# Kernel optimization log

Measured on AMD Instinct MI355X. Metric: run time of the kernel, lower is better.

## Reference

```python
import jax, jax.numpy as jnp
import numpy as np
from jax import lax


def setup_inputs() -> dict:
    key = jax.random.key(0)
    ks = jax.random.split(key, 8)
    B, L, H = 2, 1024, 2048
    E = 2
    d = H * E            # d_inner = 4096
    S = 16               # state_dim
    R = 128              # dt_rank = ceil(H / 16)
    sc = lambda fan_in: 1.0 / np.sqrt(fan_in)
    return {
        "x": jax.random.normal(ks[0], (B, L, H), jnp.float32),
        "W_in": jax.random.normal(ks[1], (H, 2 * d), jnp.float32) * sc(H),
        "conv_w": jax.random.normal(ks[2], (d, 1, 3), jnp.float32) * sc(3),
        "conv_b": jnp.zeros((d,), jnp.float32),
        "W_x": jax.random.normal(ks[3], (d, R + 2 * S), jnp.float32) * sc(d),
        "W_dt": jax.random.normal(ks[4], (R, d), jnp.float32) * sc(R),
        "b_dt": jnp.zeros((d,), jnp.float32),
        "A_log": jnp.log(jnp.tile(jnp.arange(1, S + 1, dtype=jnp.float32), (d, 1))),
        "D": jnp.ones((d,), jnp.float32),
        "W_out": jax.random.normal(ks[5], (d, H), jnp.float32) * sc(d),
    }


def reference(x, W_in, conv_w, conv_b, W_x, W_dt, b_dt, A_log, D, W_out):
    d = conv_b.shape[0]
    S = A_log.shape[1]
    R = W_dt.shape[0]
    # in_proj and gate split
    xz = x @ W_in                              # [B, L, 2d]
    xp, z = jnp.split(xz, 2, axis=-1)          # each [B, L, d]
    # depthwise conv1d (kernel 3, pad 1)
    xc = lax.conv_general_dilated(
        jnp.transpose(xp, (0, 2, 1)), conv_w, (1,), [(1, 1)],
        feature_group_count=d, dimension_numbers=("NCH", "OIH", "NCH"))
    xc = jnp.transpose(xc + conv_b[None, :, None], (0, 2, 1))  # [B, L, d]
    xc = jax.nn.silu(xc)
    # x_proj -> dt, B, C
    x_dbl = xc @ W_x                           # [B, L, R + 2S]
    dt_in = x_dbl[..., :R]
    Bm = x_dbl[..., R:R + S]                   # [B, L, S]
    Cm = x_dbl[..., R + S:]                    # [B, L, S]
    dt = jax.nn.softplus(dt_in @ W_dt + b_dt)  # [B, L, d]
    A = -jnp.exp(A_log)                        # [d, S]

    def step(h, ins):
        u_t, dt_t, B_t, C_t = ins              # [B,d], [B,d], [B,S], [B,S]
        dA = jnp.exp(dt_t[:, :, None] * A)     # [B, d, S]
        h = dA * h + dt_t[:, :, None] * B_t[:, None, :] * u_t[:, :, None]
        y_t = jnp.einsum("bds,bs->bd", h, C_t)
        return h, y_t

    h0 = jnp.zeros((x.shape[0], d, S), xc.dtype)
    xsT = (jnp.swapaxes(xc, 0, 1), jnp.swapaxes(dt, 0, 1),
           jnp.swapaxes(Bm, 0, 1), jnp.swapaxes(Cm, 0, 1))
    _, yT = lax.scan(step, h0, xsT)            # yT: [L, B, d]
    y = jnp.swapaxes(yT, 0, 1) + xc * D        # skip connection
    y = y * jax.nn.silu(z)                     # gate
    return y @ W_out                           # [B, L, H]
```

## Files before the change

### kernel.cpp

```cpp
#include <hip/hip_runtime.h>
#include <hip/hip_bf16.h>


using u16 = unsigned short;
typedef __bf16 bf16x8 __attribute__((ext_vector_type(8)));
typedef float f32x4 __attribute__((ext_vector_type(4)));
typedef u16 u16x8 __attribute__((ext_vector_type(8)));
typedef u16 u16x4 __attribute__((ext_vector_type(4)));

#define NCHUNK 16
#define CLEN   64
#define SWZ(row, q) ((q) ^ (((row) >> 1) & 3))

__device__ __forceinline__ float bf2f(u16 u) {
    union { unsigned int i; float f; } v; v.i = ((unsigned int)u) << 16; return v.f;
}
__device__ __forceinline__ u16 f2bf(float f) {
    union { float f; unsigned int i; } v; v.f = f;
    unsigned int x = v.i;
    return (u16)((x + 0x7FFFu + ((x >> 16) & 1u)) >> 16);
}

__device__ __forceinline__ float* hloc_ptr(u16* xzbase, int i) {
    return reinterpret_cast<float*>(xzbase + (size_t)(i >> 11) * 8192) + (i & 2047);
}
__device__ __forceinline__ float* hin_ptr(u16* xzbase, int i) {
    return reinterpret_cast<float*>(xzbase + (size_t)((i >> 11) + 1024) * 8192) + (i & 2047);
}

__global__ void detect_dtype(const u16* __restrict__ xraw, int* __restrict__ flag) {
    __shared__ int cnt[256];
    const int tid = threadIdx.x;
    int plausible = 0;
    for (int i = tid; i < 4096; i += 256) {
        const u16 v = xraw[2 * i];
        const int e = (v >> 7) & 0xFF;
        plausible += (e >= 100 && e <= 145) ? 1 : 0;
    }
    cnt[tid] = plausible;
    __syncthreads();
    for (int s = 128; s > 0; s >>= 1) {
        if (tid < s) cnt[tid] += cnt[tid + s];
        __syncthreads();
    }
    if (tid == 0) *flag = (cnt[0] > 2458) ? 1 : 0;
}

__device__ __forceinline__ void cvt_seg8(const void* src, u16* dst, int i8,
                                         bool isbf) {
    if (isbf) {
        *(u16x8*)&dst[i8 * 8] = *((const u16x8*)src + i8);
    } else {
        const float* f = (const float*)src + i8 * 8;
        u16x8 o;
#pragma unroll
        for (int j = 0; j < 8; j++) o[j] = f2bf(f[j]);
        *(u16x8*)&dst[i8 * 8] = o;
    }
}
__global__ void cvt_fused(const void* __restrict__ x_raw, u16* __restrict__ xcan,
                          const void* __restrict__ cw_raw, u16* __restrict__ cw_c,
                          const void* __restrict__ cb_raw, u16* __restrict__ cb_c,
                          const void* __restrict__ bdt_raw, u16* __restrict__ bdt_c,
                          const void* __restrict__ Alog_raw, u16* __restrict__ Alog_c,
                          const void* __restrict__ D_raw, u16* __restrict__ D_c,
                          const int* __restrict__ flag) {
    const bool isbf = (*flag != 0);
    int blk = blockIdx.x;
    const int tid = threadIdx.x;
    if (blk < 2048) { cvt_seg8(x_raw, xcan, blk * 256 + tid, isbf); return; }
    blk -= 2048;
    if (blk < 6)  { cvt_seg8(cw_raw, cw_c, blk * 256 + tid, isbf); return; }
    blk -= 6;
    if (blk < 2)  { cvt_seg8(cb_raw, cb_c, blk * 256 + tid, isbf); return; }
    blk -= 2;
    if (blk < 2)  { cvt_seg8(bdt_raw, bdt_c, blk * 256 + tid, isbf); return; }
    blk -= 2;
    if (blk < 32) { cvt_seg8(Alog_raw, Alog_c, blk * 256 + tid, isbf); return; }
    blk -= 32;
    cvt_seg8(D_raw, D_c, blk * 256 + tid, isbf);
}

__device__ __forceinline__ void tr_tile(const void* in, u16* out, int R, int C,
                                        int bx, int by, int tx, int ty, bool isbf,
                                        u16 (*tile)[34]) {
    const int c0 = bx * 32, r0 = by * 64;
    const int cp = tx & 15, rh = tx >> 4;
#pragma unroll
    for (int i = 0; i < 4; i++) {
        const int row = ty + rh * 8 + i * 16;
        const size_t idx = (size_t)(r0 + row) * C + c0 + cp * 2;
        if (isbf) {
            union { unsigned int u; u16 h[2]; } p;
            p.u = *reinterpret_cast<const unsigned int*>(&((const u16*)in)[idx]);
            tile[row][cp * 2] = p.h[0];
            tile[row][cp * 2 + 1] = p.h[1];
        } else {
            const float2 f = *reinterpret_cast<const float2*>(&((const float*)in)[idx]);
            tile[row][cp * 2] = f2bf(f.x);
            tile[row][cp * 2 + 1] = f2bf(f.y);
        }
    }
    __syncthreads();
#pragma unroll
    for (int i = 0; i < 4; i++) {
        const int w = ty + i * 8;
        union { u16 h[2]; unsigned int u; } p;
        p.h[0] = tile[2 * tx][w];
        p.h[1] = tile[2 * tx + 1][w];
        *reinterpret_cast<unsigned int*>(&out[(size_t)(c0 + w) * R + r0 + 2 * tx]) = p.u;
    }
}
__global__ void transpose_fused(const void* __restrict__ Wi, u16* __restrict__ WiT,
                                const void* __restrict__ Wo, u16* __restrict__ WoT,
                                const void* __restrict__ Wd, u16* __restrict__ WdT,
                                const void* __restrict__ Wx, u16* __restrict__ WxT,
                                const int* __restrict__ flag) {
    __shared__ u16 tile[64][34];
    const bool isbf = (*flag != 0);
    const int tx = threadIdx.x, ty = threadIdx.y;
    int blk = blockIdx.x;
    if (blk < 8192) { tr_tile(Wi, WiT, 2048, 8192, blk % 256, blk / 256, tx, ty, isbf, tile); return; }
    blk -= 8192;
    if (blk < 4096) { tr_tile(Wo, WoT, 4096, 2048, blk % 64, blk / 64, tx, ty, isbf, tile); return; }
    blk -= 4096;
    if (blk < 256)  { tr_tile(Wd, WdT, 128, 4096, blk % 128, blk / 128, tx, ty, isbf, tile); return; }
    blk -= 256;
    tr_tile(Wx, WxT, 4096, 160, blk % 5, blk / 5, tx, ty, isbf, tile);
}

template <int BM, int BN, int THR>
__device__ __forceinline__ void stage_ring(const u16* __restrict__ Ab,
                                           const u16* __restrict__ Bb,
                                           int K, int k0, u16* dst, int tid)
{
    constexpr int CHA = BM * 4, CHB = BN * 4;
    static_assert(CHA % THR == 0 && CHB % THR == 0, "chunk/thread mismatch");
#pragma unroll
    for (int it = 0; it < CHA / THR; it++) {
        const int c = it * THR + tid;
        const int row = c >> 2, kc = SWZ(row, c & 3);
        __builtin_amdgcn_global_load_lds(
            (const __attribute__((address_space(1))) void*)(Ab + (size_t)row * K + k0 + kc * 8),
            (__attribute__((address_space(3))) void*)(dst + c * 8), 16, 0, 0);
    }
#pragma unroll
    for (int it = 0; it < CHB / THR; it++) {
        const int c = it * THR + tid;
        const int row = c >> 2, kc = SWZ(row, c & 3);
        __builtin_amdgcn_global_load_lds(
            (const __attribute__((address_space(1))) void*)(Bb + (size_t)row * K + k0 + kc * 8),
            (__attribute__((address_space(3))) void*)(dst + BM * 32 + c * 8), 16, 0, 0);
    }
}

template <int BM, int BN, int WM, int WN, int MODE, int RING>
__global__ __launch_bounds__(64 * WM * WN, 2) void gemm_ring(
    const u16* __restrict__ A, const u16* __restrict__ Bt, void* __restrict__ C,
    const int* __restrict__ oflagp, int M, int N, int K)
{
    constexpr int THR = 64 * WM * WN;
    constexpr int MT  = BM / (WM * 16);
    constexpr int NT  = BN / (WN * 16);
    constexpr int NPH = 2;
    constexpr int GM  = MT / NPH;
    constexpr int STG = (BM + BN) * 32;
    constexpr int LPS = (BM + BN) * 4 / THR;
    constexpr int AHEAD = RING - 1;
    static_assert((BM * 4) % THR == 0 && (BN * 4) % THR == 0, "chunk split");
    static_assert(MT % NPH == 0, "MT must split into NPH phases");
    extern __shared__ u16 smem[];

    const int tid  = threadIdx.x;
    const int lane = tid & 63;
    const int wave = tid >> 6;
    const int wm = wave / WN, wn = wave % WN;
    const int q  = lane >> 4;
    const int n0 = blockIdx.x * BN;
    const int m0 = blockIdx.y * BM;
    const int Kchunk = K / gridDim.z;
    const int kbeg = blockIdx.z * Kchunk;
    const int NTILE = Kchunk >> 5;

    const u16* Ab = A  + (size_t)m0 * K + kbeg;
    const u16* Bb = Bt + (size_t)n0 * K + kbeg;

#pragma unroll
    for (int s = 0; s < AHEAD; s++)
        stage_ring<BM, BN, THR>(Ab, Bb, K, s * 32, smem + s * STG, tid);

    f32x4 acc[MT][NT];
#pragma unroll
    for (int mi = 0; mi < MT; mi++)
#pragma unroll
        for (int ni = 0; ni < NT; ni++)
            acc[mi][ni] = (f32x4){0.f, 0.f, 0.f, 0.f};

    const int arow = wm * (MT * 16) + (lane & 15);
    const int brow = wn * (NT * 16) + (lane & 15);

    int cbuf = 0;
    int pbuf = AHEAD % RING;

    for (int t = 0; t < NTILE; t++) {
        const int tp = t + AHEAD;
        if (tp < NTILE) {
            stage_ring<BM, BN, THR>(Ab, Bb, K, tp * 32, smem + pbuf * STG, tid);
            asm volatile("s_waitcnt vmcnt(%0)" :: "n"(AHEAD * LPS) : "memory");
        } else if (tp == NTILE) {
            asm volatile("s_waitcnt vmcnt(%0)" :: "n"((AHEAD - 1) * LPS) : "memory");
        } else if (tp == NTILE + 1) {
            asm volatile("s_waitcnt vmcnt(%0)" :: "n"(((AHEAD >= 2) ? (AHEAD - 2) : 0) * LPS) : "memory");
        } else {
            asm volatile("s_waitcnt vmcnt(0)" ::: "memory");
        }
        __builtin_amdgcn_s_barrier();

        const u16* As = smem + cbuf * STG;
        const u16* Bs = As + BM * 32;
        bf16x8 bfr[NT];
#pragma unroll
        for (int ni = 0; ni < NT; ni++) {
            const int r = brow + ni * 16;
            bfr[ni] = *reinterpret_cast<const bf16x8*>(&Bs[r * 32 + SWZ(r, q) * 8]);
        }
#pragma unroll
        for (int g = 0; g < NPH; g++) {
            bf16x8 af[GM];
#pragma unroll
            for (int i = 0; i < GM; i++) {
                const int r = arow + (g * GM + i) * 16;
                af[i] = *reinterpret_cast<const bf16x8*>(&As[r * 32 + SWZ(r, q) * 8]);
            }
            __builtin_amdgcn_s_setprio(1);
#pragma unroll
            for (int i = 0; i < GM; i++)
#pragma unroll
                for (int ni = 0; ni < NT; ni++)
                    acc[g * GM + i][ni] = __builtin_amdgcn_mfma_f32_16x16x32_bf16(
                        af[i], bfr[ni], acc[g * GM + i][ni], 0, 0, 0);
            __builtin_amdgcn_s_setprio(0);
            __builtin_amdgcn_sched_barrier(0);
            __builtin_amdgcn_s_barrier();
        }
        cbuf = (cbuf + 1 == RING) ? 0 : cbuf + 1;
        pbuf = (pbuf + 1 == RING) ? 0 : pbuf + 1;
    }

    int oflag = 1;
    if constexpr (MODE == 1) oflag = *oflagp;

    const int rb = m0 + wm * (MT * 16) + (q << 2);
    const int cb = n0 + wn * (NT * 16) + (lane & 15);
#pragma unroll
    for (int mi = 0; mi < MT; mi++) {
#pragma unroll
        for (int ni = 0; ni < NT; ni++) {
            const int col = cb + ni * 16;
#pragma unroll
            for (int r = 0; r < 4; r++) {
                const int row = rb + mi * 16 + r;
                const float v = acc[mi][ni][r];
                if constexpr (MODE == 0) {
                    ((u16*)C)[(size_t)row * N + col] = f2bf(v);
                } else if constexpr (MODE == 2) {
                    ((float*)C)[((size_t)blockIdx.z * M + row) * N + col] = v;
                } else {
                    if (oflag) ((u16*)C)[(size_t)row * N + col] = f2bf(v);
                    else       ((float*)C)[(size_t)row * N + col] = v;
                }
            }
        }
    }
}

__global__ void reduce_out(const float* __restrict__ part, void* __restrict__ out,
                           const int* __restrict__ flag) {
    const int idx = blockIdx.x * 256 + threadIdx.x;
    const int i4 = idx * 4;
    const float4 a = *(const float4*)&part[i4];
    const float4 b = *(const float4*)&part[(size_t)4194304 + i4];
    if (*flag) {
        u16x4 o;
        o[0] = f2bf(a.x + b.x); o[1] = f2bf(a.y + b.y);
        o[2] = f2bf(a.z + b.z); o[3] = f2bf(a.w + b.w);
        *(u16x4*)&((u16*)out)[i4] = o;
    } else {
        float4 s = {a.x + b.x, a.y + b.y, a.z + b.z, a.w + b.w};
        *(float4*)&((float*)out)[i4] = s;
    }
}

template <int BM, int BN, int BK, int WR, int WC, int MT, int NT, int MODE>
__global__ __launch_bounds__(256) void gemm_bt(
    const u16* __restrict__ A, const u16* __restrict__ Bt,
    void* __restrict__ C, const u16* __restrict__ bias,
    const int* __restrict__ oflagp,
    int M, int N, int K)
{
    static_assert(BK == 32, "BK=32 (one 16x16x32 MFMA k-slab)");
    __shared__ u16 As[BM * BK];
    __shared__ u16 Bs[BN * BK];

    const int tid  = threadIdx.x;
    const int lane = tid & 63;
    const int wave = tid >> 6;
    const int wm = wave / WC, wn = wave % WC;

    const int m0 = blockIdx.y * BM;
    const int n0 = blockIdx.x * BN;
    const int Kchunk = K / gridDim.z;
    const int kbeg = blockIdx.z * Kchunk;
    const int kend = kbeg + Kchunk;

    f32x4 acc[MT][NT];
#pragma unroll
    for (int mi = 0; mi < MT; mi++)
#pragma unroll
        for (int ni = 0; ni < NT; ni++)
            acc[mi][ni] = (f32x4){0.f, 0.f, 0.f, 0.f};

    const int q = lane >> 4;
    const int arow = wm * MT * 16 + (lane & 15);
    const int brow = wn * NT * 16 + (lane & 15);

    constexpr int CHA = BM * 4;
    constexpr int CHB = BN * 4;

    for (int k0 = kbeg; k0 < kend; k0 += BK) {
        __syncthreads();
#pragma unroll
        for (int it = 0; it < (CHA + 255) / 256; it++) {
            const int c = it * 256 + tid;
            if (CHA % 256 == 0 || c < CHA) {
                const int row = c >> 2, kc = SWZ(row, c & 3);
                const u16* gp = &A[(size_t)(m0 + row) * K + k0 + kc * 8];
                __builtin_amdgcn_global_load_lds(
                    (const __attribute__((address_space(1))) void*)gp,
                    (__attribute__((address_space(3))) void*)&As[c * 8], 16, 0, 0);
            }
        }
#pragma unroll
        for (int it = 0; it < (CHB + 255) / 256; it++) {
            const int c = it * 256 + tid;
            if (CHB % 256 == 0 || c < CHB) {
                const int row = c >> 2, kc = SWZ(row, c & 3);
                const u16* gp = &Bt[(size_t)(n0 + row) * K + k0 + kc * 8];
                __builtin_amdgcn_global_load_lds(
                    (const __attribute__((address_space(1))) void*)gp,
                    (__attribute__((address_space(3))) void*)&Bs[c * 8], 16, 0, 0);
            }
        }
        __syncthreads();

        bf16x8 af[MT], bfr[NT];
#pragma unroll
        for (int mi = 0; mi < MT; mi++) {
            const int row = arow + mi * 16;
            af[mi] = *reinterpret_cast<const bf16x8*>(&As[row * BK + SWZ(row, q) * 8]);
        }
#pragma unroll
        for (int ni = 0; ni < NT; ni++) {
            const int row = brow + ni * 16;
            bfr[ni] = *reinterpret_cast<const bf16x8*>(&Bs[row * BK + SWZ(row, q) * 8]);
        }
#pragma unroll
        for (int mi = 0; mi < MT; mi++)
#pragma unroll
            for (int ni = 0; ni < NT; ni++)
                acc[mi][ni] = __builtin_amdgcn_mfma_f32_16x16x32_bf16(
                    af[mi], bfr[ni], acc[mi][ni], 0, 0, 0);
    }

    const int rb = m0 + wm * MT * 16 + ((lane >> 4) << 2);
    const int cb = n0 + wn * NT * 16 + (lane & 15);
#pragma unroll
    for (int mi = 0; mi < MT; mi++) {
#pragma unroll
        for (int ni = 0; ni < NT; ni++) {
            const int col = cb + ni * 16;
#pragma unroll
            for (int r = 0; r < 4; r++) {
                const int row = rb + mi * 16 + r;
                const float v = acc[mi][ni][r];
                if constexpr (MODE == 0) {
                    ((u16*)C)[(size_t)row * N + col] = f2bf(v);
                } else if constexpr (MODE == 5) {
                    ((float*)C)[((size_t)blockIdx.z * M + row) * N + col] = v;
                }
            }
        }
    }
}

__global__ void reduce_xdbl(const float* __restrict__ part,
                            float* __restrict__ x_dbl, u16* __restrict__ dtin) {
    const int idx = blockIdx.x * 256 + threadIdx.x;
    const int row = idx / 160, col = idx - row * 160;
    float s = 0.f;
#pragma unroll
    for (int z = 0; z < 16; z++) s += part[(size_t)z * (2048 * 160) + idx];
    x_dbl[idx] = s;
    if (col < 128) dtin[row * 128 + col] = f2bf(s);
}

__global__ __launch_bounds__(256) void dt_gemm(
    const u16* __restrict__ A,
    const u16* __restrict__ Bt,
    u16* __restrict__ C,
    const u16* __restrict__ bias)
{
    __shared__ ulong4 smem_raw[2048];
    u16* As = (u16*)smem_raw;
    u16* Bs = As + 64 * 128;
    float* Cs = (float*)smem_raw;

    const int tid  = threadIdx.x;
    const int lane = tid & 63;
    const int wave = tid >> 6;
    const int n0 = blockIdx.x * 64;
    const int m0 = blockIdx.y * 64;

#pragma unroll
    for (int it = 0; it < 4; it++) {
        const int c = it * 256 + tid;
        const int row = c >> 4, cc = (c & 15) ^ (row & 7);
        const u16* gp = &A[(size_t)(m0 + row) * 128 + cc * 8];
        __builtin_amdgcn_global_load_lds(
            (const __attribute__((address_space(1))) void*)gp,
            (__attribute__((address_space(3))) void*)&As[c * 8], 16, 0, 0);
    }
#pragma unroll
    for (int it = 0; it < 4; it++) {
        const int c = it * 256 + tid;
        const int row = c >> 4, cc = (c & 15) ^ (row & 7);
        const u16* gp = &Bt[(size_t)(n0 + row) * 128 + cc * 8];
        __builtin_amdgcn_global_load_lds(
            (const __attribute__((address_space(1))) void*)gp,
            (__attribute__((address_space(3))) void*)&Bs[c * 8], 16, 0, 0);
    }
    __syncthreads();

    const int q  = lane >> 4;
    const int ar = wave * 16 + (lane & 15);
    f32x4 acc[4];
#pragma unroll
    for (int ni = 0; ni < 4; ni++) acc[ni] = (f32x4){0.f, 0.f, 0.f, 0.f};

#pragma unroll
    for (int kk = 0; kk < 4; kk++) {
        const int cA = kk * 4 + q;
        const bf16x8 af = *reinterpret_cast<const bf16x8*>(
            &As[(ar * 16 + (cA ^ (ar & 7))) * 8]);
#pragma unroll
        for (int ni = 0; ni < 4; ni++) {
            const int br = ni * 16 + (lane & 15);
            const bf16x8 bfr = *reinterpret_cast<const bf16x8*>(
                &Bs[(br * 16 + (cA ^ (br & 7))) * 8]);
            acc[ni] = __builtin_amdgcn_mfma_f32_16x16x32_bf16(af, bfr, acc[ni], 0, 0, 0);
        }
    }
    __syncthreads();

#pragma unroll
    for (int ni = 0; ni < 4; ni++) {
        const int col = ni * 16 + (lane & 15);
#pragma unroll
        for (int r = 0; r < 4; r++) {
            const int rowl = wave * 16 + q * 4 + r;
            Cs[rowl * 68 + col] = acc[ni][r];
        }
    }
    __syncthreads();

#pragma unroll
    for (int p = 0; p < 4; p++) {
        const int rowl = p * 16 + (tid >> 4);
        const int c0 = (tid & 15) * 4;
        float4 v = *reinterpret_cast<const float4*>(&Cs[rowl * 68 + c0]);
        float* vp = reinterpret_cast<float*>(&v);
        u16x4 o;
#pragma unroll
        for (int j = 0; j < 4; j++) {
            const float x = vp[j] + bf2f(bias[n0 + c0 + j]);
            o[j] = f2bf(fmaxf(x, 0.f) + __logf(1.f + __expf(-fabsf(x))));
        }
        *reinterpret_cast<u16x4*>(&C[(size_t)(m0 + rowl) * 4096 + n0 + c0]) = o;
    }
}

__global__ void conv_silu(const u16* __restrict__ xz, const u16* __restrict__ conv_w,
                          const u16* __restrict__ conv_b, u16* __restrict__ xc) {
    const int idx = blockIdx.x * 256 + threadIdx.x;
    const int row = idx >> 9, c0 = (idx & 511) * 8;
    const int l = row & 1023;

    u16 wcat[24];
    *(u16x8*)&wcat[0]  = *(const u16x8*)&conv_w[c0 * 3];
    *(u16x8*)&wcat[8]  = *(const u16x8*)&conv_w[c0 * 3 + 8];
    *(u16x8*)&wcat[16] = *(const u16x8*)&conv_w[c0 * 3 + 16];
    const u16x8 bv = *(const u16x8*)&conv_b[c0];
    const u16x8 x0 = *(const u16x8*)&xz[(size_t)row * 8192 + c0];
    u16x8 xm = {}, xp = {};
    if (l > 0)    xm = *(const u16x8*)&xz[(size_t)(row - 1) * 8192 + c0];
    if (l < 1023) xp = *(const u16x8*)&xz[(size_t)(row + 1) * 8192 + c0];

    u16x8 out;
#pragma unroll
    for (int i = 0; i < 8; i++) {
        float v = bf2f(wcat[3 * i]) * bf2f(xm[i])
                + bf2f(wcat[3 * i + 1]) * bf2f(x0[i])
                + bf2f(wcat[3 * i + 2]) * bf2f(xp[i])
                + bf2f(bv[i]);
        v = v / (1.f + __expf(-v));
        out[i] = f2bf(v);
    }
    *(u16x8*)&xc[(size_t)row * 4096 + c0] = out;
}

__global__ __launch_bounds__(256) void scan_p1(
    const u16* __restrict__ dt, const u16* __restrict__ xc,
    const float* __restrict__ x_dbl, const u16* __restrict__ A_log,
    float* __restrict__ Parr, u16* __restrict__ xzbase)
{
    __shared__ float Bsm[CLEN][16];
    const int tid = threadIdx.x;
    const int nc = blockIdx.x, cg = blockIdx.y, b = blockIdx.z;
    const int ch = cg * 256 + tid;
    const size_t row0 = (size_t)b * 1024 + nc * CLEN;

    {
        const int t = tid >> 2, q = tid & 3;
        const float4 v = *(const float4*)&x_dbl[(row0 + t) * 160 + 128 + q * 4];
        *(float4*)&Bsm[t][q * 4] = v;
    }
    __syncthreads();

    float A_s[16], h[16];
#pragma unroll
    for (int s = 0; s < 16; s++) {
        A_s[s] = -__expf(bf2f(A_log[ch * 16 + s]));
        h[s] = 0.f;
    }
    float Sdt = 0.f;

    float dt_v = bf2f(dt[row0 * 4096 + ch]);
    float u_v  = bf2f(xc[row0 * 4096 + ch]);
    for (int t = 0; t < CLEN; t++) {
        const int tn = (t + 1 < CLEN) ? t + 1 : t;
        const float dt_n = bf2f(dt[(row0 + tn) * 4096 + ch]);
        const float u_n  = bf2f(xc[(row0 + tn) * 4096 + ch]);
        const float dtu = dt_v * u_v;
        Sdt += dt_v;
        const f32x4* Brow = (const f32x4*)&Bsm[t][0];
        const f32x4 B0 = Brow[0], B1 = Brow[1], B2 = Brow[2], B3 = Brow[3];
#pragma unroll
        for (int s = 0; s < 16; s++) {
            const float Bs_ = (s < 4 ? B0[s & 3] : s < 8 ? B1[s & 3] : s < 12 ? B2[s & 3] : B3[s & 3]);
            const float dA = __expf(dt_v * A_s[s]);
            h[s] = dA * h[s] + dtu * Bs_;
        }
        dt_v = dt_n; u_v = u_n;
    }
    const int i0 = (((b * NCHUNK + nc) * 4096) + ch) * 16;
    float* pp = &Parr[i0];
    float* hp = hloc_ptr(xzbase, i0);
#pragma unroll
    for (int s4 = 0; s4 < 4; s4++) {
        float4 pq, hq;
        pq.x = __expf(A_s[4 * s4 + 0] * Sdt);
        pq.y = __expf(A_s[4 * s4 + 1] * Sdt);
        pq.z = __expf(A_s[4 * s4 + 2] * Sdt);
        pq.w = __expf(A_s[4 * s4 + 3] * Sdt);
        hq.x = h[4 * s4 + 0]; hq.y = h[4 * s4 + 1];
        hq.z = h[4 * s4 + 2]; hq.w = h[4 * s4 + 3];
        *(float4*)&pp[4 * s4] = pq;
        *(float4*)&hp[4 * s4] = hq;
    }
}

__global__ __launch_bounds__(256) void scan_p2(
    const float* __restrict__ Parr, u16* __restrict__ xzbase)
{
    const int tid = threadIdx.x;
    const int lane = tid & 63, wave = tid >> 6;
    const int blk = blockIdx.x;
    const int b = blk >> 8, cg = blk & 255;
    const int c_local = lane & 3, s = lane >> 2;
    const int ch = cg * 16 + wave * 4 + c_local;

    float Pv[NCHUNK], hl[NCHUNK];
#pragma unroll
    for (int c = 0; c < NCHUNK; c++) {
        const int i = (((b * NCHUNK + c) * 4096) + ch) * 16 + s;
        Pv[c] = Parr[i];
        hl[c] = *hloc_ptr(xzbase, i);
    }
    float hin = 0.f;
#pragma unroll
    for (int c = 0; c < NCHUNK; c++) {
        const int i = (((b * NCHUNK + c) * 4096) + ch) * 16 + s;
        *hin_ptr(xzbase, i) = hin;
        hin = Pv[c] * hin + hl[c];
    }
}

__global__ __launch_bounds__(256) void scan_p3(
    const u16* __restrict__ dt, const u16* __restrict__ xc,
    const float* __restrict__ x_dbl, const u16* __restrict__ xz,
    const u16* __restrict__ A_log, const u16* __restrict__ Dp,
    u16* __restrict__ yg, u16* __restrict__ xzbase)
{
    __shared__ float BCs[CLEN][32];
    const int tid = threadIdx.x;
    const int nc = blockIdx.x, cg = blockIdx.y, b = blockIdx.z;
    const int ch = cg * 256 + tid;
    const size_t row0 = (size_t)b * 1024 + nc * CLEN;

#pragma unroll
    for (int it = 0; it < 2; it++) {
        const int c = it * 256 + tid;
        const int t = c >> 3, q = c & 7;
        const float4 v = *(const float4*)&x_dbl[(row0 + t) * 160 + 128 + q * 4];
        *(float4*)&BCs[t][q * 4] = v;
    }
    __syncthreads();

    float A_s[16], h[16];
    const int i0 = (((b * NCHUNK + nc) * 4096) + ch) * 16;
    {
        const float* hp = hin_ptr(xzbase, i0);
#pragma unroll
        for (int s4 = 0; s4 < 4; s4++) {
            const float4 hq = *(const float4*)&hp[4 * s4];
            h[4 * s4 + 0] = hq.x; h[4 * s4 + 1] = hq.y;
            h[4 * s4 + 2] = hq.z; h[4 * s4 + 3] = hq.w;
        }
    }
#pragma unroll
    for (int s = 0; s < 16; s++)
        A_s[s] = -__expf(bf2f(A_log[ch * 16 + s]));
    const float D_ch = bf2f(Dp[ch]);

    float dt_v = bf2f(dt[row0 * 4096 + ch]);
    float u_v  = bf2f(xc[row0 * 4096 + ch]);
    float z_v  = bf2f(xz[row0 * 8192 + 4096 + ch]);
    for (int t = 0; t < CLEN; t++) {
        const int tn = (t + 1 < CLEN) ? t + 1 : t;
        const size_t rn = row0 + tn;
        const float dt_n = bf2f(dt[rn * 4096 + ch]);
        const float u_n  = bf2f(xc[rn * 4096 + ch]);
        const float z_n  = bf2f(xz[rn * 8192 + 4096 + ch]);
        const float dtu = dt_v * u_v;

        const f32x4* Row = (const f32x4*)&BCs[t][0];
        const f32x4 B0 = Row[0], B1 = Row[1], B2 = Row[2], B3 = Row[3];
        const f32x4 C0 = Row[4], C1 = Row[5], C2 = Row[6], C3 = Row[7];

        float y0 = 0.f, y1 = 0.f, y2 = 0.f, y3 = 0.f;
#pragma unroll
        for (int s = 0; s < 16; s++) {
            const float Bs_ = (s < 4 ? B0[s & 3] : s < 8 ? B1[s & 3] : s < 12 ? B2[s & 3] : B3[s & 3]);
            const float Cs_ = (s < 4 ? C0[s & 3] : s < 8 ? C1[s & 3] : s < 12 ? C2[s & 3] : C3[s & 3]);
            const float dA = __expf(dt_v * A_s[s]);
            h[s] = dA * h[s] + dtu * Bs_;
            const float hc = h[s] * Cs_;
            if ((s & 3) == 0) y0 += hc; else if ((s & 3) == 1) y1 += hc;
            else if ((s & 3) == 2) y2 += hc; else y3 += hc;
        }
        const float y = (y0 + y1) + (y2 + y3);
        const float silu_z = z_v / (1.f + __expf(-z_v));
        yg[(row0 + t) * 4096 + ch] = f2bf((y + u_v * D_ch) * silu_z);
        dt_v = dt_n; u_v = u_n; z_v = z_n;
    }
}

extern "C" void kernel_launch(void* const* d_in, const int* in_sizes, int n_in,
                              void* d_out, int out_size, void* d_ws, size_t ws_size,
                              hipStream_t stream)
{
    const void* x_raw      = d_in[0];
    const void* W_in_raw   = d_in[1];
    const void* conv_w_raw = d_in[2];
    const void* conv_b_raw = d_in[3];
    const void* W_x_raw    = d_in[4];
    const void* W_dt_raw   = d_in[5];
    const void* b_dt_raw   = d_in[6];
    const void* A_log_raw  = d_in[7];
    const void* D_raw      = d_in[8];
    const void* W_out_raw  = d_in[9];

    char* ws = (char*)d_ws;
    size_t off = 0;
    auto alloc = [&](size_t bytes) { char* p = ws + off; off += (bytes + 255) & ~(size_t)255; return p; };
    int*   flag   = (int*)  alloc(4);
    u16*   W_inT  = (u16*)  alloc(8192ULL * 2048 * 2);
    u16*   W_outT = (u16*)  alloc(2048ULL * 4096 * 2);
    u16*   W_dtT  = (u16*)  alloc(4096ULL * 128 * 2);
    u16*   W_xT   = (u16*)  alloc(160ULL * 4096 * 2);
    u16*   xz     = (u16*)  alloc(2048ULL * 8192 * 2);
    u16*   xc     = (u16*)  alloc(2048ULL * 4096 * 2);
    float* x_dbl  = (float*)alloc(2048ULL * 160 * 4);
    u16*   dtin   = (u16*)  alloc(2048ULL * 128 * 2);
    u16*   yg     = (u16*)  alloc(2048ULL * 4096 * 2);
    u16*   xcan   = (u16*)  alloc(2048ULL * 2048 * 2);
    float* xdblp  = (float*)alloc(16ULL * 2048 * 160 * 4);
    u16*   cw_c   = (u16*)  alloc(12288 * 2);
    u16*   cb_c   = (u16*)  alloc(4096 * 2);
    u16*   bdt_c  = (u16*)  alloc(4096 * 2);
    u16*   Alog_c = (u16*)  alloc(65536 * 2);
    u16*   D_c    = (u16*)  alloc(4096 * 2);
    u16*   dtv    = (u16*)W_inT;
    float* Parr   = (float*)xcan;
    float* outp   = (float*)W_inT;

    detect_dtype<<<1, 256, 0, stream>>>((const u16*)x_raw, flag);
    cvt_fused<<<2048 + 6 + 2 + 2 + 32 + 2, 256, 0, stream>>>(
        x_raw, xcan, conv_w_raw, cw_c, conv_b_raw, cb_c, b_dt_raw, bdt_c,
        A_log_raw, Alog_c, D_raw, D_c, flag);

    transpose_fused<<<8192 + 4096 + 256 + 320, dim3(32, 8), 0, stream>>>(
        W_in_raw, W_inT, W_out_raw, W_outT, W_dt_raw, W_dtT, W_x_raw, W_xT, flag);

    (void)hipFuncSetAttribute(
        reinterpret_cast<const void*>(&gemm_ring<256, 128, 2, 2, 0, 3>),
        hipFuncAttributeMaxDynamicSharedMemorySize, 73728);
    gemm_ring<256, 128, 2, 2, 0, 3><<<dim3(8192 / 128, 2048 / 256, 1), 256, 73728, stream>>>(
        xcan, W_inT, xz, nullptr, 2048, 8192, 2048);

    conv_silu<<<(2048 * 512) / 256, 256, 0, stream>>>(xz, cw_c, cb_c, xc);

    gemm_bt<64, 160, 32, 4, 1, 1, 10, 5>
        <<<dim3(1, 2048 / 64, 16), 256, 0, stream>>>(xc, W_xT, xdblp, nullptr, nullptr, 2048, 160, 4096);

    reduce_xdbl<<<(2048 * 160) / 256, 256, 0, stream>>>(xdblp, x_dbl, dtin);

    dt_gemm<<<dim3(4096 / 64, 2048 / 64), 256, 0, stream>>>(dtin, W_dtT, dtv, bdt_c);

    scan_p1<<<dim3(NCHUNK, 16, 2), 256, 0, stream>>>(dtv, xc, x_dbl, Alog_c, Parr, xz);
    scan_p2<<<512, 256, 0, stream>>>(Parr, xz);
    scan_p3<<<dim3(NCHUNK, 16, 2), 256, 0, stream>>>(dtv, xc, x_dbl, xz, Alog_c, D_c, yg, xz);

    (void)hipFuncSetAttribute(
        reinterpret_cast<const void*>(&gemm_ring<128, 128, 2, 2, 2, 4>),
        hipFuncAttributeMaxDynamicSharedMemorySize, 65536);
    gemm_ring<128, 128, 2, 2, 2, 4><<<dim3(2048 / 128, 2048 / 128, 2), 256, 65536, stream>>>(
        yg, W_outT, outp, nullptr, 2048, 2048, 4096);
    reduce_out<<<(2048 * 2048 / 4) / 256, 256, 0, stream>>>(outp, d_out, flag);
}
```

Measured before the change: 408.5 us.

## Fuse prep kernels, merge scan passes, and drop split-K in output GEMM

Combines dtype detection, input conversion and weight transposes into one prep kernel using a ballot-based detection. Merges scan pass 2 into pass 3 by having each chunk recompute its incoming state from earlier chunk summaries. Removes split-K from the output projection so it writes the final output directly, eliminating the reduce kernel and fp32 partial buffer. This trades launch and memory-traffic savings for redundant carry work and fewer blocks in the final GEMM.

```diff
diff --git a/kernel.cpp b/kernel.cpp
--- a/kernel.cpp
+++ b/kernel.cpp
@@ -24,26 +24,8 @@
 __device__ __forceinline__ float* hloc_ptr(u16* xzbase, int i) {
     return reinterpret_cast<float*>(xzbase + (size_t)(i >> 11) * 8192) + (i & 2047);
 }
-__device__ __forceinline__ float* hin_ptr(u16* xzbase, int i) {
-    return reinterpret_cast<float*>(xzbase + (size_t)((i >> 11) + 1024) * 8192) + (i & 2047);
-}
-
-__global__ void detect_dtype(const u16* __restrict__ xraw, int* __restrict__ flag) {
-    __shared__ int cnt[256];
-    const int tid = threadIdx.x;
-    int plausible = 0;
-    for (int i = tid; i < 4096; i += 256) {
-        const u16 v = xraw[2 * i];
-        const int e = (v >> 7) & 0xFF;
-        plausible += (e >= 100 && e <= 145) ? 1 : 0;
-    }
-    cnt[tid] = plausible;
-    __syncthreads();
-    for (int s = 128; s > 0; s >>= 1) {
-        if (tid < s) cnt[tid] += cnt[tid + s];
-        __syncthreads();
-    }
-    if (tid == 0) *flag = (cnt[0] > 2458) ? 1 : 0;
+__device__ __forceinline__ const float* hloc_cptr(const u16* xzbase, int i) {
+    return reinterpret_cast<const float*>(xzbase + (size_t)(i >> 11) * 8192) + (i & 2047);
 }
 
 __device__ __forceinline__ void cvt_seg8(const void* src, u16* dst, int i8,
@@ -57,28 +39,6 @@
         for (int j = 0; j < 8; j++) o[j] = f2bf(f[j]);
         *(u16x8*)&dst[i8 * 8] = o;
     }
-}
-__global__ void cvt_fused(const void* __restrict__ x_raw, u16* __restrict__ xcan,
-                          const void* __restrict__ cw_raw, u16* __restrict__ cw_c,
-                          const void* __restrict__ cb_raw, u16* __restrict__ cb_c,
-                          const void* __restrict__ bdt_raw, u16* __restrict__ bdt_c,
-                          const void* __restrict__ Alog_raw, u16* __restrict__ Alog_c,
-                          const void* __restrict__ D_raw, u16* __restrict__ D_c,
-                          const int* __restrict__ flag) {
-    const bool isbf = (*flag != 0);
-    int blk = blockIdx.x;
-    const int tid = threadIdx.x;
-    if (blk < 2048) { cvt_seg8(x_raw, xcan, blk * 256 + tid, isbf); return; }
-    blk -= 2048;
-    if (blk < 6)  { cvt_seg8(cw_raw, cw_c, blk * 256 + tid, isbf); return; }
-    blk -= 6;
-    if (blk < 2)  { cvt_seg8(cb_raw, cb_c, blk * 256 + tid, isbf); return; }
-    blk -= 2;
-    if (blk < 2)  { cvt_seg8(bdt_raw, bdt_c, blk * 256 + tid, isbf); return; }
-    blk -= 2;
-    if (blk < 32) { cvt_seg8(Alog_raw, Alog_c, blk * 256 + tid, isbf); return; }
-    blk -= 32;
-    cvt_seg8(D_raw, D_c, blk * 256 + tid, isbf);
 }
 
 __device__ __forceinline__ void tr_tile(const void* in, u16* out, int R, int C,
@@ -111,15 +71,47 @@
         *reinterpret_cast<unsigned int*>(&out[(size_t)(c0 + w) * R + r0 + 2 * tx]) = p.u;
     }
 }
-__global__ void transpose_fused(const void* __restrict__ Wi, u16* __restrict__ WiT,
-                                const void* __restrict__ Wo, u16* __restrict__ WoT,
-                                const void* __restrict__ Wd, u16* __restrict__ WdT,
-                                const void* __restrict__ Wx, u16* __restrict__ WxT,
-                                const int* __restrict__ flag) {
+
+__global__ void prep_fused(const void* __restrict__ x_raw, u16* __restrict__ xcan,
+                           const void* __restrict__ cw_raw, u16* __restrict__ cw_c,
+                           const void* __restrict__ cb_raw, u16* __restrict__ cb_c,
+                           const void* __restrict__ bdt_raw, u16* __restrict__ bdt_c,
+                           const void* __restrict__ Alog_raw, u16* __restrict__ Alog_c,
+                           const void* __restrict__ D_raw, u16* __restrict__ D_c,
+                           const void* __restrict__ Wi, u16* __restrict__ WiT,
+                           const void* __restrict__ Wo, u16* __restrict__ WoT,
+                           const void* __restrict__ Wd, u16* __restrict__ WdT,
+                           const void* __restrict__ Wx, u16* __restrict__ WxT,
+                           int* __restrict__ flag) {
     __shared__ u16 tile[64][34];
-    const bool isbf = (*flag != 0);
-    const int tx = threadIdx.x, ty = threadIdx.y;
+    __shared__ int ws4[4];
+    const int tid = threadIdx.x;
+
+    {
+        const u16 v = ((const u16*)x_raw)[2 * (tid * 16)];
+        const int e = (v >> 7) & 0xFF;
+        const unsigned long long m = __ballot(e >= 100 && e <= 145);
+        if ((tid & 63) == 0) ws4[tid >> 6] = __popcll(m);
+    }
+    __syncthreads();
+    const bool isbf = (ws4[0] + ws4[1] + ws4[2] + ws4[3]) > 153;
+    if (blockIdx.x == 0 && tid == 0) *flag = isbf ? 1 : 0;
+    __syncthreads();
+
     int blk = blockIdx.x;
+    if (blk < 2048) { cvt_seg8(x_raw, xcan, blk * 256 + tid, isbf); return; }
+    blk -= 2048;
+    if (blk < 6)  { cvt_seg8(cw_raw, cw_c, blk * 256 + tid, isbf); return; }
+    blk -= 6;
+    if (blk < 2)  { cvt_seg8(cb_raw, cb_c, blk * 256 + tid, isbf); return; }
+    blk -= 2;
+    if (blk < 2)  { cvt_seg8(bdt_raw, bdt_c, blk * 256 + tid, isbf); return; }
+    blk -= 2;
+    if (blk < 32) { cvt_seg8(Alog_raw, Alog_c, blk * 256 + tid, isbf); return; }
+    blk -= 32;
+    if (blk < 2)  { cvt_seg8(D_raw, D_c, blk * 256 + tid, isbf); return; }
+    blk -= 2;
+    const int tx = tid & 31, ty = tid >> 5;
     if (blk < 8192) { tr_tile(Wi, WiT, 2048, 8192, blk % 256, blk / 256, tx, ty, isbf, tile); return; }
     blk -= 8192;
     if (blk < 4096) { tr_tile(Wo, WoT, 4096, 2048, blk % 64, blk / 64, tx, ty, isbf, tile); return; }
@@ -178,12 +170,10 @@
     const int q  = lane >> 4;
     const int n0 = blockIdx.x * BN;
     const int m0 = blockIdx.y * BM;
-    const int Kchunk = K / gridDim.z;
-    const int kbeg = blockIdx.z * Kchunk;
-    const int NTILE = Kchunk >> 5;
-
-    const u16* Ab = A  + (size_t)m0 * K + kbeg;
-    const u16* Bb = Bt + (size_t)n0 * K + kbeg;
+    const int NTILE = K >> 5;
+
+    const u16* Ab = A  + (size_t)m0 * K;
+    const u16* Bb = Bt + (size_t)n0 * K;
 
 #pragma unroll
     for (int s = 0; s < AHEAD; s++)
@@ -263,31 +253,12 @@
                 const float v = acc[mi][ni][r];
                 if constexpr (MODE == 0) {
                     ((u16*)C)[(size_t)row * N + col] = f2bf(v);
-                } else if constexpr (MODE == 2) {
-                    ((float*)C)[((size_t)blockIdx.z * M + row) * N + col] = v;
                 } else {
                     if (oflag) ((u16*)C)[(size_t)row * N + col] = f2bf(v);
                     else       ((float*)C)[(size_t)row * N + col] = v;
                 }
             }
         }
-    }
-}
-
-__global__ void reduce_out(const float* __restrict__ part, void* __restrict__ out,
-                           const int* __restrict__ flag) {
-    const int idx = blockIdx.x * 256 + threadIdx.x;
-    const int i4 = idx * 4;
-    const float4 a = *(const float4*)&part[i4];
-    const float4 b = *(const float4*)&part[(size_t)4194304 + i4];
-    if (*flag) {
-        u16x4 o;
-        o[0] = f2bf(a.x + b.x); o[1] = f2bf(a.y + b.y);
-        o[2] = f2bf(a.z + b.z); o[3] = f2bf(a.w + b.w);
-        *(u16x4*)&((u16*)out)[i4] = o;
-    } else {
-        float4 s = {a.x + b.x, a.y + b.y, a.z + b.z, a.w + b.w};
-        *(float4*)&((float*)out)[i4] = s;
     }
 }
 
@@ -579,37 +550,12 @@
     }
 }
 
-__global__ __launch_bounds__(256) void scan_p2(
-    const float* __restrict__ Parr, u16* __restrict__ xzbase)
-{
-    const int tid = threadIdx.x;
-    const int lane = tid & 63, wave = tid >> 6;
-    const int blk = blockIdx.x;
-    const int b = blk >> 8, cg = blk & 255;
-    const int c_local = lane & 3, s = lane >> 2;
-    const int ch = cg * 16 + wave * 4 + c_local;
-
-    float Pv[NCHUNK], hl[NCHUNK];
-#pragma unroll
-    for (int c = 0; c < NCHUNK; c++) {
-        const int i = (((b * NCHUNK + c) * 4096) + ch) * 16 + s;
-        Pv[c] = Parr[i];
-        hl[c] = *hloc_ptr(xzbase, i);
-    }
-    float hin = 0.f;
-#pragma unroll
-    for (int c = 0; c < NCHUNK; c++) {
-        const int i = (((b * NCHUNK + c) * 4096) + ch) * 16 + s;
-        *hin_ptr(xzbase, i) = hin;
-        hin = Pv[c] * hin + hl[c];
-    }
-}
-
-__global__ __launch_bounds__(256) void scan_p3(
+__global__ __launch_bounds__(256) void scan_p23(
     const u16* __restrict__ dt, const u16* __restrict__ xc,
     const float* __restrict__ x_dbl, const u16* __restrict__ xz,
     const u16* __restrict__ A_log, const u16* __restrict__ Dp,
-    u16* __restrict__ yg, u16* __restrict__ xzbase)
+    u16* __restrict__ yg, const float* __restrict__ Parr,
+    const u16* __restrict__ xzbase)
 {
     __shared__ float BCs[CLEN][32];
     const int tid = threadIdx.x;
@@ -627,21 +573,28 @@
     __syncthreads();
 
     float A_s[16], h[16];
-    const int i0 = (((b * NCHUNK + nc) * 4096) + ch) * 16;
-    {
-        const float* hp = hin_ptr(xzbase, i0);
+#pragma unroll
+    for (int s = 0; s < 16; s++) {
+        A_s[s] = -__expf(bf2f(A_log[ch * 16 + s]));
+        h[s] = 0.f;
+    }
+
+    for (int c = 0; c < nc; c++) {
+        const int ib = (((b * NCHUNK + c) * 4096) + ch) * 16;
+        const float* pp = &Parr[ib];
+        const float* hp = hloc_cptr(xzbase, ib);
 #pragma unroll
         for (int s4 = 0; s4 < 4; s4++) {
-            const float4 hq = *(const float4*)&hp[4 * s4];
-            h[4 * s4 + 0] = hq.x; h[4 * s4 + 1] = hq.y;
-            h[4 * s4 + 2] = hq.z; h[4 * s4 + 3] = hq.w;
-        }
-    }
-#pragma unroll
-    for (int s = 0; s < 16; s++)
-        A_s[s] = -__expf(bf2f(A_log[ch * 16 + s]));
+            const float4 P4 = *(const float4*)&pp[4 * s4];
+            const float4 H4 = *(const float4*)&hp[4 * s4];
+            h[4 * s4 + 0] = P4.x * h[4 * s4 + 0] + H4.x;
+            h[4 * s4 + 1] = P4.y * h[4 * s4 + 1] + H4.y;
+            h[4 * s4 + 2] = P4.z * h[4 * s4 + 2] + H4.z;
+            h[4 * s4 + 3] = P4.w * h[4 * s4 + 3] + H4.w;
+        }
+    }
+
     const float D_ch = bf2f(Dp[ch]);
-
     float dt_v = bf2f(dt[row0 * 4096 + ch]);
     float u_v  = bf2f(xc[row0 * 4096 + ch]);
     float z_v  = bf2f(xz[row0 * 8192 + 4096 + ch]);
@@ -712,14 +665,10 @@
     u16*   D_c    = (u16*)  alloc(4096 * 2);
     u16*   dtv    = (u16*)W_inT;
     float* Parr   = (float*)xcan;
-    float* outp   = (float*)W_inT;
-
-    detect_dtype<<<1, 256, 0, stream>>>((const u16*)x_raw, flag);
-    cvt_fused<<<2048 + 6 + 2 + 2 + 32 + 2, 256, 0, stream>>>(
+
+    prep_fused<<<2092 + 12864, 256, 0, stream>>>(
         x_raw, xcan, conv_w_raw, cw_c, conv_b_raw, cb_c, b_dt_raw, bdt_c,
-        A_log_raw, Alog_c, D_raw, D_c, flag);
-
-    transpose_fused<<<8192 + 4096 + 256 + 320, dim3(32, 8), 0, stream>>>(
+        A_log_raw, Alog_c, D_raw, D_c,
         W_in_raw, W_inT, W_out_raw, W_outT, W_dt_raw, W_dtT, W_x_raw, W_xT, flag);
 
     (void)hipFuncSetAttribute(
@@ -738,13 +687,12 @@
     dt_gemm<<<dim3(4096 / 64, 2048 / 64), 256, 0, stream>>>(dtin, W_dtT, dtv, bdt_c);
 
     scan_p1<<<dim3(NCHUNK, 16, 2), 256, 0, stream>>>(dtv, xc, x_dbl, Alog_c, Parr, xz);
-    scan_p2<<<512, 256, 0, stream>>>(Parr, xz);
-    scan_p3<<<dim3(NCHUNK, 16, 2), 256, 0, stream>>>(dtv, xc, x_dbl, xz, Alog_c, D_c, yg, xz);
+    scan_p23<<<dim3(NCHUNK, 16, 2), 256, 0, stream>>>(
+        dtv, xc, x_dbl, xz, Alog_c, D_c, yg, Parr, xz);
 
     (void)hipFuncSetAttribute(
-        reinterpret_cast<const void*>(&gemm_ring<128, 128, 2, 2, 2, 4>),
+        reinterpret_cast<const void*>(&gemm_ring<128, 128, 2, 2, 1, 4>),
         hipFuncAttributeMaxDynamicSharedMemorySize, 65536);
-    gemm_ring<128, 128, 2, 2, 2, 4><<<dim3(2048 / 128, 2048 / 128, 2), 256, 65536, stream>>>(
-        yg, W_outT, outp, nullptr, 2048, 2048, 4096);
-    reduce_out<<<(2048 * 2048 / 4) / 256, 256, 0, stream>>>(outp, d_out, flag);
-}
+    gemm_ring<128, 128, 2, 2, 1, 4><<<dim3(2048 / 128, 2048 / 128, 1), 256, 65536, stream>>>(
+        yg, W_outT, d_out, flag, 2048, 2048, 4096);
+}
```

Measured after the change: 415.6 us. About the same (+1.7%).
